# Performance work log

Measured on AMD Instinct MI355X. Metric: run time of the kernel, lower is better.

Reference implementation:

```python
import jax, jax.numpy as jnp
import numpy as np

C = 192; G = 12; CG = C // G          # channels, groups, channels per group
KS = 3; PAD = 1; K = KS * KS - 1      # 3x3 kernel, remove_center=True -> 8 points
HID = 4 * C                           # mlp_ratio = 4
OFFSET_SCALE = 1.0

# kernel dilation grid (x, y) pairs, center removed (remove_center=True)
_pts = np.arange(KS) - (KS - 1) // 2
_gx, _gy = np.meshgrid(_pts, _pts, indexing='ij')
_grid = np.stack([_gx.ravel(), _gy.ravel()], -1).astype(np.float32)
_grid = _grid[~np.all(_grid == 0, axis=1)]   # (K, 2)
GRID = jnp.asarray(_grid)


def _ln(x, w, b, eps=1e-5):
    mu = jnp.mean(x, -1, keepdims=True)
    var = jnp.var(x, -1, keepdims=True)
    return (x - mu) * jax.lax.rsqrt(var + eps) * w + b


def _dcnv3(x, in_proj_w, in_proj_b, dw_w, dw_b, dw_ln_w, dw_ln_b,
           off_w, off_b, mask_w, mask_b, cfs_w, cfs_b, out_proj_w, out_proj_b):
    # x: (B, H, W, C) channels-last
    B, H, W, _ = x.shape
    xp = x @ in_proj_w + in_proj_b          # value / x_proj
    # depthwise conv -> LN -> GELU on the raw input (offset/mask branch)
    x1 = jax.lax.conv_general_dilated(
        x, dw_w, (1, 1), 'SAME',
        dimension_numbers=('NHWC', 'HWIO', 'NHWC'),
        feature_group_count=C) + dw_b
    x1 = jax.nn.gelu(_ln(x1, dw_ln_w, dw_ln_b, 1e-6), approximate=False)
    off = (x1 @ off_w + off_b).reshape(B, H, W, G, K, 2)      # (dx, dy) in pixels
    mask = jax.nn.softmax((x1 @ mask_w + mask_b).reshape(B, H, W, G, K), axis=-1)
    # pad value and flatten spatial; (B, Hp*Wp, G, 1, CG)
    Hp, Wp = H + 2 * PAD, W + 2 * PAD
    v = jnp.pad(xp, ((0, 0), (PAD, PAD), (PAD, PAD), (0, 0))).reshape(B, Hp * Wp, G, 1, CG)
    # sampling locations in padded-image pixel index coords (grid_sample align_corners=False)
    bx = jnp.arange(W, dtype=x.dtype)[None, None, :, None, None] + PAD
    by = jnp.arange(H, dtype=x.dtype)[None, :, None, None, None] + PAD
    px = (bx + (GRID[:, 0] + off[..., 0]) * OFFSET_SCALE).reshape(B, H * W, G, K)
    py = (by + (GRID[:, 1] + off[..., 1]) * OFFSET_SCALE).reshape(B, H * W, G, K)
    x0 = jnp.floor(px); y0 = jnp.floor(py)
    wx = px - x0; wy = py - y0
    ix0 = x0.astype(jnp.int32); iy0 = y0.astype(jnp.int32)

    def gather(iy, ix):
        valid = ((iy >= 0) & (iy < Hp) & (ix >= 0) & (ix < Wp)).astype(x.dtype)
        idx = jnp.clip(iy, 0, Hp - 1) * Wp + jnp.clip(ix, 0, Wp - 1)
        s = jnp.take_along_axis(v, idx[..., None], axis=1)    # (B, HW, G, K, CG)
        return s * valid[..., None]

    s = (gather(iy0, ix0)         * ((1 - wy) * (1 - wx))[..., None]
       + gather(iy0, ix0 + 1)     * ((1 - wy) * wx)[..., None]
       + gather(iy0 + 1, ix0)     * (wy * (1 - wx))[..., None]
       + gather(iy0 + 1, ix0 + 1) * (wy * wx)[..., None])
    out = jnp.einsum('bngk,bngkc->bngc', mask.reshape(B, H * W, G, K), s).reshape(B, H, W, C)
    # center feature scale
    cfs = jax.nn.sigmoid(x1 @ cfs_w.T + cfs_b)                # (B, H, W, G)
    cfs = jnp.repeat(cfs, CG, axis=-1)                        # (B, H, W, C)
    out = out * (1 - cfs) + xp * cfs
    return out @ out_proj_w + out_proj_b


def _forward(x, norm1_w, norm1_b, norm2_w, norm2_b, rpn1_w, rpn1_b, rpn2_w, rpn2_b,
             in_proj_w, in_proj_b, dw_w, dw_b, dw_ln_w, dw_ln_b, off_w, off_b,
             mask_w, mask_b, cfs_w, cfs_b, out_proj_w, out_proj_b,
             fc1_w, fc1_b, fc2_w, fc2_b):
    d = _dcnv3(_ln(x, norm1_w, norm1_b), in_proj_w, in_proj_b, dw_w, dw_b,
               dw_ln_w, dw_ln_b, off_w, off_b, mask_w, mask_b, cfs_w, cfs_b,
               out_proj_w, out_proj_b)
    x = x + _ln(d, rpn1_w, rpn1_b)                            # res_post_norm branch 1
    h = jax.nn.gelu(_ln(x, norm2_w, norm2_b) @ fc1_w + fc1_b, approximate=False) @ fc2_w + fc2_b
    x = x + _ln(h, rpn2_w, rpn2_b)                            # res_post_norm branch 2
    return x


def setup_inputs():
    key = jax.random.key(0)
    ks = jax.random.split(key, 12)
    r = lambda i, shape, s=0.02: jax.random.normal(ks[i], shape, jnp.float32) * s
    B, H, W = 4, 56, 56
    return dict(
        x=jax.random.normal(ks[0], (B, H, W, C), jnp.float32),
        norm1_w=jnp.ones((C,)), norm1_b=jnp.zeros((C,)),
        norm2_w=jnp.ones((C,)), norm2_b=jnp.zeros((C,)),
        rpn1_w=jnp.ones((C,)), rpn1_b=jnp.zeros((C,)),
        rpn2_w=jnp.ones((C,)), rpn2_b=jnp.zeros((C,)),
        in_proj_w=r(1, (C, C)), in_proj_b=jnp.zeros((C,)),
        dw_w=r(2, (KS, KS, 1, C), 0.1), dw_b=jnp.zeros((C,)),
        dw_ln_w=jnp.ones((C,)), dw_ln_b=jnp.zeros((C,)),
        off_w=r(3, (C, G * K * 2), 0.1), off_b=jnp.zeros((G * K * 2,)),
        mask_w=r(4, (C, G * K), 0.1), mask_b=jnp.zeros((G * K,)),
        cfs_w=r(5, (G, C), 0.1), cfs_b=jnp.zeros((G,)),
        out_proj_w=r(6, (C, C)), out_proj_b=jnp.zeros((C,)),
        fc1_w=r(7, (C, HID)), fc1_b=jnp.zeros((HID,)),
        fc2_w=r(8, (HID, C)), fc2_b=jnp.zeros((C,)),
    )


def reference(x, norm1_w, norm1_b, norm2_w, norm2_b, rpn1_w, rpn1_b, rpn2_w, rpn2_b,
              in_proj_w, in_proj_b, dw_w, dw_b, dw_ln_w, dw_ln_b, off_w, off_b,
              mask_w, mask_b, cfs_w, cfs_b, out_proj_w, out_proj_b,
              fc1_w, fc1_b, fc2_w, fc2_b):
    return _forward(x, norm1_w, norm1_b, norm2_w, norm2_b, rpn1_w, rpn1_b, rpn2_w, rpn2_b,
                    in_proj_w, in_proj_b, dw_w, dw_b, dw_ln_w, dw_ln_b, off_w, off_b,
                    mask_w, mask_b, cfs_w, cfs_b, out_proj_w, out_proj_b,
                    fc1_w, fc1_b, fc2_w, fc2_b)
```

## Files before the change

### kernel.cpp

```cpp
#include <hip/hip_runtime.h>
#include <hip/hip_bf16.h>
#include <math.h>


#define BATCH 4
#define HH 56
#define WW 56
#define CC 192
#define NPIX (BATCH * HH * WW)
#define XS_STR 200
#define H1S 776
#define OFS 193
#define MLS 97

typedef __hip_bfloat16 bf16;
typedef __attribute__((ext_vector_type(8))) short short8;
typedef __attribute__((ext_vector_type(4))) float float4v;

__device__ __forceinline__ float gelu_exact(float x) {
    return 0.5f * x * (1.f + erff(x * 0.70710678118654752f));
}
__device__ __forceinline__ bf16 f2b(float f) { return __float2bfloat16(f); }
__device__ __forceinline__ float b2f(bf16 h) { return __bfloat162float(h); }
__device__ __forceinline__ float4 ldb4(const bf16* p) {
    const ushort4 u = *(const ushort4*)p;
    float4 r;
    r.x = __uint_as_float((unsigned)u.x << 16);
    r.y = __uint_as_float((unsigned)u.y << 16);
    r.z = __uint_as_float((unsigned)u.z << 16);
    r.w = __uint_as_float((unsigned)u.w << 16);
    return r;
}
__device__ __forceinline__ void stb4(bf16* p, float4 v) {
    ushort4 u;
    bf16 h;
    h = f2b(v.x); u.x = *(unsigned short*)&h;
    h = f2b(v.y); u.y = *(unsigned short*)&h;
    h = f2b(v.z); u.z = *(unsigned short*)&h;
    h = f2b(v.w); u.w = *(unsigned short*)&h;
    *(ushort4*)p = u;
}

__global__ __launch_bounds__(256) void prep_w_k(const float* __restrict__ inpw,
        const float* __restrict__ offw, const float* __restrict__ maskw,
        const float* __restrict__ outpw, const float* __restrict__ fc1w,
        const float* __restrict__ fc2w, bf16* __restrict__ wsB)
{
    const int i = blockIdx.x * 256 + threadIdx.x;
    bf16* inpP = wsB;
    bf16* omP  = wsB + 36864;
    bf16* outP = wsB + 92160;
    bf16* fc1P = wsB + 129024;
    bf16* fc2P = wsB + 276480;
    const int j   = i & 7;
    const int l   = (i >> 3) & 63;
    const int n15 = l & 15, q = l >> 4;
    const int grp = i >> 9;
    if (i < 36864) {
        const int t = grp / 6, c = grp - t * 6;
        const int n = 16 * t + n15, k = 32 * c + 8 * q + j;
        inpP[i] = f2b(inpw[(size_t)k * 192 + n]);
        outP[i] = f2b(outpw[(size_t)k * 192 + n]);
    }
    if (i < 55296) {
        const int t = grp / 6, c = grp - t * 6;
        const int n = 16 * t + n15, k = 32 * c + 8 * q + j;
        omP[i] = (n < 192) ? f2b(offw[(size_t)k * 192 + n])
                           : f2b(maskw[(size_t)k * 96 + (n - 192)]);
    }
    if (i < 147456) {
        const int t1 = grp / 6, c1 = grp - t1 * 6;
        const int n1 = 16 * t1 + n15, k1 = 32 * c1 + 8 * q + j;
        fc1P[i] = f2b(fc1w[(size_t)k1 * 768 + n1]);
        const int t2 = grp / 24, c2 = grp - t2 * 24;
        const int n2 = 16 * t2 + n15, k2 = 32 * c2 + 8 * q + j;
        fc2P[i] = f2b(fc2w[(size_t)k2 * 192 + n2]);
    }
}

__global__ __launch_bounds__(256) void ln_gemm16_k(const float* __restrict__ x,
        const float* __restrict__ n1w, const float* __restrict__ n1b,
        const bf16* __restrict__ wP, const float* __restrict__ bias,
        bf16* __restrict__ xn_out, bf16* __restrict__ xp_out)
{
    __shared__ __align__(16) bf16 xs[16 * XS_STR];
    const int tid = threadIdx.x;
    const int w   = tid >> 6;
    const int l   = tid & 63;
    const int n15 = l & 15;
    const int q   = l >> 4;
    const int p0  = blockIdx.x * 16;

    #pragma unroll
    for (int rr = 0; rr < 4; rr++) {
        const int lr = 4 * w + rr;
        const size_t base = (size_t)(p0 + lr) * CC;
        float v[3];
        #pragma unroll
        for (int i = 0; i < 3; i++) v[i] = x[base + l + 64 * i];
        float s = v[0] + v[1] + v[2];
        float qq = v[0]*v[0] + v[1]*v[1] + v[2]*v[2];
        #pragma unroll
        for (int off = 32; off > 0; off >>= 1) {
            s  += __shfl_xor(s, off, 64);
            qq += __shfl_xor(qq, off, 64);
        }
        const float mu  = s * (1.f / CC);
        const float var = qq * (1.f / CC) - mu * mu;
        const float rs  = rsqrtf(var + 1e-5f);
        #pragma unroll
        for (int i = 0; i < 3; i++) {
            const int c = l + 64 * i;
            const bf16 h = f2b((v[i] - mu) * rs * n1w[c] + n1b[c]);
            xs[lr * XS_STR + c] = h;
            xn_out[base + c] = h;
        }
    }
    __syncthreads();

    short8 aF[6];
    #pragma unroll
    for (int c = 0; c < 6; c++)
        aF[c] = *(const short8*)&xs[n15 * XS_STR + c * 32 + q * 8];

    #pragma unroll
    for (int t = 0; t < 3; t++) {
        const int tile = 3 * w + t;
        float4v acc = (float4v){0.f, 0.f, 0.f, 0.f};
        #pragma unroll
        for (int c = 0; c < 6; c++) {
            const short8 bF = *(const short8*)&wP[(size_t)((tile * 6 + c) * 64 + l) * 8];
            acc = __builtin_amdgcn_mfma_f32_16x16x32_bf16(aF[c], bF, acc, 0, 0, 0);
        }
        const int n0 = 16 * tile;
        const float bb = bias[n0 + n15];
        #pragma unroll
        for (int r = 0; r < 4; r++)
            xp_out[(size_t)(p0 + 4 * q + r) * 192 + n0 + n15] = f2b(acc[r] + bb);
    }
}

__global__ __launch_bounds__(256) void dwconv_ln_gelu_k(
        const bf16* __restrict__ xn, const float* __restrict__ dww,
        const float* __restrict__ dwb, const float* __restrict__ lnw,
        const float* __restrict__ lnb, bf16* __restrict__ x1)
{
    __shared__ float cv[4][192];
    const int bid  = (blockIdx.x & 7) * (NPIX / 32) + (blockIdx.x >> 3);
    const int t    = threadIdx.x;
    const int ws   = t >> 6;
    const int l    = t & 63;
    const int pix  = bid * 4 + ws;
    const int bimg = pix / (HH * WW);
    const int hw   = pix - bimg * HH * WW;
    const int h    = hw / WW;
    const int wx   = hw - h * WW;

    if (l < 48) {
        const int c0 = l * 4;
        float4 acc = *(const float4*)&dwb[c0];
        #pragma unroll
        for (int ky = 0; ky < 3; ky++) {
            const int yy = h + ky - 1;
            if (yy < 0 || yy >= HH) continue;
            #pragma unroll
            for (int kx = 0; kx < 3; kx++) {
                const int xx = wx + kx - 1;
                if (xx < 0 || xx >= WW) continue;
                const float4 a = ldb4(&xn[((size_t)(bimg * HH + yy) * WW + xx) * CC + c0]);
                const float4 ww = *(const float4*)&dww[(ky * 3 + kx) * CC + c0];
                acc.x += a.x * ww.x; acc.y += a.y * ww.y;
                acc.z += a.z * ww.z; acc.w += a.w * ww.w;
            }
        }
        *(float4*)&cv[ws][c0] = acc;
    }
    __syncthreads();

    float v[3];
    #pragma unroll
    for (int i = 0; i < 3; i++) v[i] = cv[ws][l + 64 * i];
    float s = v[0] + v[1] + v[2];
    float q = v[0]*v[0] + v[1]*v[1] + v[2]*v[2];
    #pragma unroll
    for (int off = 32; off > 0; off >>= 1) {
        s += __shfl_xor(s, off, 64);
        q += __shfl_xor(q, off, 64);
    }
    const float mu  = s * (1.f / CC);
    const float var = q * (1.f / CC) - mu * mu;
    const float rs  = rsqrtf(var + 1e-6f);
    #pragma unroll
    for (int i = 0; i < 3; i++) {
        const int c = l + 64 * i;
        x1[(size_t)pix * CC + c] = f2b(gelu_exact((v[i] - mu) * rs * lnw[c] + lnb[c]));
    }
}

__global__ __launch_bounds__(256) void offmask_sample_k(
        const bf16* __restrict__ xp, const bf16* __restrict__ x1g,
        const bf16* __restrict__ omP, const float* __restrict__ offb,
        const float* __restrict__ maskb, const float* __restrict__ cfsw,
        const float* __restrict__ cfsb, bf16* __restrict__ outb)
{
    __shared__ __align__(16) bf16 xs[8 * XS_STR];
    __shared__ float offs_l[8][OFS];
    __shared__ float mls_l[8][MLS];

    const int tid = threadIdx.x;
    const int w   = tid >> 6;
    const int l   = tid & 63;
    const int n15 = l & 15;
    const int q   = l >> 4;
    const int bid = (blockIdx.x & 7) * (NPIX / 64) + (blockIdx.x >> 3);
    const int p0  = bid * 8;

    for (int i = tid; i < 8 * 24; i += 256) {
        const int px = i / 24, c8 = i - px * 24;
        *(short8*)&xs[px * XS_STR + c8 * 8] = *(const short8*)&x1g[(size_t)(p0 + px) * 192 + c8 * 8];
    }
    __syncthreads();

    {
        short8 aF[6];
        #pragma unroll
        for (int c = 0; c < 6; c++)
            aF[c] = (n15 < 8)
                  ? *(const short8*)&xs[n15 * XS_STR + c * 32 + q * 8]
                  : (short8){0, 0, 0, 0, 0, 0, 0, 0};

        for (int t = w; t < 18; t += 4) {
            float4v acc = (float4v){0.f, 0.f, 0.f, 0.f};
            #pragma unroll
            for (int c = 0; c < 6; c++) {
                const short8 bF = *(const short8*)&omP[(size_t)((t * 6 + c) * 64 + l) * 8];
                acc = __builtin_amdgcn_mfma_f32_16x16x32_bf16(aF[c], bF, acc, 0, 0, 0);
            }
            if (q < 2) {
                const int n0 = 16 * t;
                if (t < 12) {
                    const float bb = offb[n0 + n15];
                    #pragma unroll
                    for (int r = 0; r < 4; r++)
                        offs_l[4 * q + r][n0 + n15] = acc[r] + bb;
                } else {
                    const int m0 = n0 - 192;
                    const float bb = maskb[m0 + n15];
                    #pragma unroll
                    for (int r = 0; r < 4; r++)
                        mls_l[4 * q + r][m0 + n15] = acc[r] + bb;
                }
            }
        }
    }
    __syncthreads();

    #pragma unroll
    for (int it = 0; it < 2; it++) {
        const int id = tid + 256 * it;
        if (id >= 384) break;
        const int px  = id / 48;
        const int s2  = id - px * 48;
        const int g   = s2 >> 2;
        const int c4  = s2 & 3;
        const int ch0 = g * 16 + c4 * 4;
        const int pix = p0 + px;
        const int bimg = pix / (HH * WW);
        const int hw   = pix - bimg * HH * WW;
        const int h    = hw / WW;
        const int wxp  = hw - h * WW;

        float lg[8];
        float mx = -1e30f;
        #pragma unroll
        for (int k = 0; k < 8; k++) { lg[k] = mls_l[px][g * 8 + k]; mx = fmaxf(mx, lg[k]); }
        float se = 0.f;
        #pragma unroll
        for (int k = 0; k < 8; k++) { lg[k] = expf(lg[k] - mx); se += lg[k]; }
        const float inv = 1.f / se;

        const int GX[8] = {-1, -1, -1, 0, 0, 1, 1, 1};
        const int GY[8] = {-1, 0, 1, -1, 1, -1, 0, 1};
        const size_t imgbase = (size_t)bimg * HH * WW * CC;

        float4 acc = {0.f, 0.f, 0.f, 0.f};
        #pragma unroll 2
        for (int k = 0; k < 8; k++) {
            const float px_ = (float)wxp + (float)GX[k] + offs_l[px][g * 16 + 2 * k];
            const float py_ = (float)h   + (float)GY[k] + offs_l[px][g * 16 + 2 * k + 1];
            const float fx = floorf(px_), fy = floorf(py_);
            const float wxf = px_ - fx, wyf = py_ - fy;
            const int x0 = (int)fx, y0 = (int)fy;
            float4 v00 = {0,0,0,0}, v01 = {0,0,0,0}, v10 = {0,0,0,0}, v11 = {0,0,0,0};
            if (y0 >= 0 && y0 < HH) {
                if (x0 >= 0 && x0 < WW)
                    v00 = ldb4(&xp[imgbase + (size_t)(y0 * WW + x0) * CC + ch0]);
                if (x0 + 1 >= 0 && x0 + 1 < WW)
                    v01 = ldb4(&xp[imgbase + (size_t)(y0 * WW + x0 + 1) * CC + ch0]);
            }
            if (y0 + 1 >= 0 && y0 + 1 < HH) {
                if (x0 >= 0 && x0 < WW)
                    v10 = ldb4(&xp[imgbase + (size_t)((y0 + 1) * WW + x0) * CC + ch0]);
                if (x0 + 1 >= 0 && x0 + 1 < WW)
                    v11 = ldb4(&xp[imgbase + (size_t)((y0 + 1) * WW + x0 + 1) * CC + ch0]);
            }
            const float w00 = (1.f - wyf) * (1.f - wxf), w01 = (1.f - wyf) * wxf;
            const float w10 = wyf * (1.f - wxf),         w11 = wyf * wxf;
            const float mk = lg[k] * inv;
            acc.x += mk * (w00 * v00.x + w01 * v01.x + w10 * v10.x + w11 * v11.x);
            acc.y += mk * (w00 * v00.y + w01 * v01.y + w10 * v10.y + w11 * v11.y);
            acc.z += mk * (w00 * v00.z + w01 * v01.z + w10 * v10.z + w11 * v11.z);
            acc.w += mk * (w00 * v00.w + w01 * v01.w + w10 * v10.w + w11 * v11.w);
        }

        float part = 0.f;
        #pragma unroll
        for (int j = 0; j < 48; j++)
            part += b2f(xs[px * XS_STR + 4 * j + c4]) * cfsw[(size_t)g * CC + 4 * j + c4];
        part += __shfl_xor(part, 1, 64);
        part += __shfl_xor(part, 2, 64);
        const float cf = 1.f / (1.f + expf(-(part + cfsb[g])));

        const float4 xpc = ldb4(&xp[(size_t)pix * CC + ch0]);
        float4 o;
        o.x = acc.x * (1.f - cf) + xpc.x * cf;
        o.y = acc.y * (1.f - cf) + xpc.y * cf;
        o.z = acc.z * (1.f - cf) + xpc.z * cf;
        o.w = acc.w * (1.f - cf) + xpc.w * cf;
        stb4(&outb[(size_t)pix * CC + ch0], o);
    }
}

__global__ __launch_bounds__(256) void gemm_ln2_mlp_k(const bf16* __restrict__ A,
        const bf16* __restrict__ wP, const float* __restrict__ bias,
        const float* __restrict__ x,
        const float* __restrict__ r1w, const float* __restrict__ r1b,
        const float* __restrict__ n2w, const float* __restrict__ n2b,
        const bf16* __restrict__ fc1P, const float* __restrict__ fc1b,
        const bf16* __restrict__ fc2P, const float* __restrict__ fc2b,
        const float* __restrict__ r2w, const float* __restrict__ r2b,
        float* __restrict__ out)
{
    __shared__ __align__(16) bf16 xs[16 * XS_STR];
    __shared__ __align__(16) bf16 h1[16 * H1S];
    __shared__ float ps[4][16], pq[4][16], ps2[4][16], pq2[4][16];

    const int tid = threadIdx.x;
    const int w   = tid >> 6;
    const int l   = tid & 63;
    const int n15 = l & 15;
    const int q   = l >> 4;
    const int p0  = blockIdx.x * 16;

    for (int i = tid; i < 16 * 24; i += 256) {
        const int px = i / 24, c8 = i - px * 24;
        *(short8*)&xs[px * XS_STR + c8 * 8] = *(const short8*)&A[(size_t)(p0 + px) * 192 + c8 * 8];
    }
    __syncthreads();

    {
        short8 aF[6];
        #pragma unroll
        for (int c = 0; c < 6; c++)
            aF[c] = *(const short8*)&xs[n15 * XS_STR + c * 32 + q * 8];

        float4v acc[3];
        #pragma unroll
        for (int t = 0; t < 3; t++) {
            const int tile = 3 * w + t;
            acc[t] = (float4v){0.f, 0.f, 0.f, 0.f};
            #pragma unroll
            for (int c = 0; c < 6; c++) {
                const short8 bF = *(const short8*)&wP[(size_t)((tile * 6 + c) * 64 + l) * 8];
                acc[t] = __builtin_amdgcn_mfma_f32_16x16x32_bf16(aF[c], bF, acc[t], 0, 0, 0);
            }
            const float bb = bias[16 * tile + n15];
            #pragma unroll
            for (int r = 0; r < 4; r++) acc[t][r] += bb;
        }

        #pragma unroll
        for (int r = 0; r < 4; r++) {
            float sp = acc[0][r] + acc[1][r] + acc[2][r];
            float qp = acc[0][r]*acc[0][r] + acc[1][r]*acc[1][r] + acc[2][r]*acc[2][r];
            #pragma unroll
            for (int o = 1; o < 16; o <<= 1) {
                sp += __shfl_xor(sp, o, 64);
                qp += __shfl_xor(qp, o, 64);
            }
            if (n15 == 0) { ps[w][4 * q + r] = sp; pq[w][4 * q + r] = qp; }
        }
        __syncthreads();

        float x2v[3][4];
        #pragma unroll
        for (int r = 0; r < 4; r++) {
            const int row = 4 * q + r;
            const float s  = ps[0][row] + ps[1][row] + ps[2][row] + ps[3][row];
            const float qq = pq[0][row] + pq[1][row] + pq[2][row] + pq[3][row];
            const float mu  = s * (1.f / CC);
            const float var = qq * (1.f / CC) - mu * mu;
            const float rs  = rsqrtf(var + 1e-5f);
            const size_t grow = p0 + row;
            #pragma unroll
            for (int t = 0; t < 3; t++) {
                const int col = 48 * w + 16 * t + n15;
                x2v[t][r] = x[grow * CC + col] + (acc[t][r] - mu) * rs * r1w[col] + r1b[col];
            }
        }
        #pragma unroll
        for (int r = 0; r < 4; r++) {
            float sp = x2v[0][r] + x2v[1][r] + x2v[2][r];
            float qp = x2v[0][r]*x2v[0][r] + x2v[1][r]*x2v[1][r] + x2v[2][r]*x2v[2][r];
            #pragma unroll
            for (int o = 1; o < 16; o <<= 1) {
                sp += __shfl_xor(sp, o, 64);
                qp += __shfl_xor(qp, o, 64);
            }
            if (n15 == 0) { ps2[w][4 * q + r] = sp; pq2[w][4 * q + r] = qp; }
        }
        __syncthreads();

        #pragma unroll
        for (int r = 0; r < 4; r++) {
            const int row = 4 * q + r;
            const float s  = ps2[0][row] + ps2[1][row] + ps2[2][row] + ps2[3][row];
            const float qq = pq2[0][row] + pq2[1][row] + pq2[2][row] + pq2[3][row];
            const float mu  = s * (1.f / CC);
            const float var = qq * (1.f / CC) - mu * mu;
            const float rs  = rsqrtf(var + 1e-5f);
            #pragma unroll
            for (int t = 0; t < 3; t++) {
                const int col = 48 * w + 16 * t + n15;
                xs[row * XS_STR + col] = f2b((x2v[t][r] - mu) * rs * n2w[col] + n2b[col]);
            }
        }
        __syncthreads();

        short8 aF2[6];
        #pragma unroll
        for (int c = 0; c < 6; c++)
            aF2[c] = *(const short8*)&xs[n15 * XS_STR + c * 32 + q * 8];

        #pragma unroll
        for (int t1 = 0; t1 < 12; t1++) {
            const int tile = 12 * w + t1;
            float4v a1 = (float4v){0.f, 0.f, 0.f, 0.f};
            #pragma unroll
            for (int c = 0; c < 6; c++) {
                const short8 bF = *(const short8*)&fc1P[(size_t)((tile * 6 + c) * 64 + l) * 8];
                a1 = __builtin_amdgcn_mfma_f32_16x16x32_bf16(aF2[c], bF, a1, 0, 0, 0);
            }
            const int n0 = 16 * tile;
            const float bb = fc1b[n0 + n15];
            #pragma unroll
            for (int r = 0; r < 4; r++)
                h1[(4 * q + r) * H1S + n0 + n15] = f2b(gelu_exact(a1[r] + bb));
        }
        __syncthreads();

        float4v acc2[3];
        #pragma unroll
        for (int t = 0; t < 3; t++) acc2[t] = (float4v){0.f, 0.f, 0.f, 0.f};
        #pragma unroll 4
        for (int kc = 0; kc < 24; kc++) {
            const short8 a2 = *(const short8*)&h1[n15 * H1S + kc * 32 + q * 8];
            #pragma unroll
            for (int t = 0; t < 3; t++) {
                const int tile = 3 * w + t;
                const short8 bF = *(const short8*)&fc2P[(size_t)((tile * 24 + kc) * 64 + l) * 8];
                acc2[t] = __builtin_amdgcn_mfma_f32_16x16x32_bf16(a2, bF, acc2[t], 0, 0, 0);
            }
        }
        #pragma unroll
        for (int t = 0; t < 3; t++) {
            const float bb = fc2b[48 * w + 16 * t + n15];
            #pragma unroll
            for (int r = 0; r < 4; r++) acc2[t][r] += bb;
        }

        #pragma unroll
        for (int r = 0; r < 4; r++) {
            float sp = acc2[0][r] + acc2[1][r] + acc2[2][r];
            float qp = acc2[0][r]*acc2[0][r] + acc2[1][r]*acc2[1][r] + acc2[2][r]*acc2[2][r];
            #pragma unroll
            for (int o = 1; o < 16; o <<= 1) {
                sp += __shfl_xor(sp, o, 64);
                qp += __shfl_xor(qp, o, 64);
            }
            if (n15 == 0) { ps[w][4 * q + r] = sp; pq[w][4 * q + r] = qp; }
        }
        __syncthreads();

        #pragma unroll
        for (int r = 0; r < 4; r++) {
            const int row = 4 * q + r;
            const float s  = ps[0][row] + ps[1][row] + ps[2][row] + ps[3][row];
            const float qq = pq[0][row] + pq[1][row] + pq[2][row] + pq[3][row];
            const float mu  = s * (1.f / CC);
            const float var = qq * (1.f / CC) - mu * mu;
            const float rs  = rsqrtf(var + 1e-5f);
            const size_t grow = p0 + row;
            #pragma unroll
            for (int t = 0; t < 3; t++) {
                const int col = 48 * w + 16 * t + n15;
                out[grow * CC + col] = x2v[t][r]
                                     + (acc2[t][r] - mu) * rs * r2w[col] + r2b[col];
            }
        }
    }
}

extern "C" void kernel_launch(void* const* d_in, const int* in_sizes, int n_in,
                              void* d_out, int out_size, void* d_ws, size_t ws_size,
                              hipStream_t stream) {
    const float* x      = (const float*)d_in[0];
    const float* n1w    = (const float*)d_in[1];
    const float* n1b    = (const float*)d_in[2];
    const float* n2w    = (const float*)d_in[3];
    const float* n2b    = (const float*)d_in[4];
    const float* rpn1w  = (const float*)d_in[5];
    const float* rpn1b  = (const float*)d_in[6];
    const float* rpn2w  = (const float*)d_in[7];
    const float* rpn2b  = (const float*)d_in[8];
    const float* inpw   = (const float*)d_in[9];
    const float* inpb   = (const float*)d_in[10];
    const float* dww    = (const float*)d_in[11];
    const float* dwb    = (const float*)d_in[12];
    const float* dwlnw  = (const float*)d_in[13];
    const float* dwlnb  = (const float*)d_in[14];
    const float* offw   = (const float*)d_in[15];
    const float* offb   = (const float*)d_in[16];
    const float* maskw  = (const float*)d_in[17];
    const float* maskb  = (const float*)d_in[18];
    const float* cfsw   = (const float*)d_in[19];
    const float* cfsb   = (const float*)d_in[20];
    const float* outpw  = (const float*)d_in[21];
    const float* outpb  = (const float*)d_in[22];
    const float* fc1w   = (const float*)d_in[23];
    const float* fc1b   = (const float*)d_in[24];
    const float* fc2w   = (const float*)d_in[25];
    const float* fc2b   = (const float*)d_in[26];

    const int N = NPIX;
    const size_t NP = (size_t)N * CC;
    bf16* B0  = (bf16*)d_ws;
    bf16* B1  = B0 + NP;
    bf16* B3  = B1 + NP;
    bf16* wsB = B3 + NP;
    const bf16* inpP = wsB;
    const bf16* omP  = wsB + 36864;
    const bf16* outP = wsB + 92160;
    const bf16* fc1P = wsB + 129024;
    const bf16* fc2P = wsB + 276480;

    const int lnG = N / 4;
    const int g16 = N / 16;
    const int g8  = N / 8;

    prep_w_k<<<576, 256, 0, stream>>>(inpw, offw, maskw, outpw, fc1w, fc2w, wsB);
    ln_gemm16_k<<<g16, 256, 0, stream>>>(x, n1w, n1b, inpP, inpb, B0, B1);
    dwconv_ln_gelu_k<<<lnG, 256, 0, stream>>>(B0, dww, dwb, dwlnw, dwlnb, B3);
    offmask_sample_k<<<g8, 256, 0, stream>>>(B1, B3, omP, offb, maskb,
                                             cfsw, cfsb, B0);
    gemm_ln2_mlp_k<<<g16, 256, 0, stream>>>(B0, outP, outpb, x, rpn1w, rpn1b,
                                            n2w, n2b, fc1P, fc1b, fc2P, fc2b,
                                            rpn2w, rpn2b, (float*)d_out);
}
```

Before: 210.6 us.

## Fold center-feature-scale into offset/mask MFMA and widen sampling loads to 8 channels

Appends the 12 center-feature-scale weight columns as an extra MFMA tile in the packed offset/mask weight, so the sigmoid gate is computed by the matrix unit instead of a scalar 48-term dot product per thread. Softmax over mask logits moves into the MFMA epilogue using lane shuffles, so the normalized mask is stored in shared memory. The bilinear sampling phase now has each thread handle 8 channels with 16-byte loads, using 192 threads instead of 384 thread-slots. This cuts redundant scalar work and load instructions, at the cost of fewer active threads and more registers per thread in the gather loop.

```diff
diff --git a/kernel.cpp b/kernel.cpp
--- a/kernel.cpp
+++ b/kernel.cpp
@@ -22,6 +22,9 @@
 }
 __device__ __forceinline__ bf16 f2b(float f) { return __float2bfloat16(f); }
 __device__ __forceinline__ float b2f(bf16 h) { return __bfloat162float(h); }
+__device__ __forceinline__ float b2fu(short s) {
+    return __uint_as_float((unsigned)(unsigned short)s << 16);
+}
 __device__ __forceinline__ float4 ldb4(const bf16* p) {
     const ushort4 u = *(const ushort4*)p;
     float4 r;
@@ -43,15 +46,16 @@
 
 __global__ __launch_bounds__(256) void prep_w_k(const float* __restrict__ inpw,
         const float* __restrict__ offw, const float* __restrict__ maskw,
-        const float* __restrict__ outpw, const float* __restrict__ fc1w,
-        const float* __restrict__ fc2w, bf16* __restrict__ wsB)
+        const float* __restrict__ cfsw, const float* __restrict__ outpw,
+        const float* __restrict__ fc1w, const float* __restrict__ fc2w,
+        bf16* __restrict__ wsB)
 {
     const int i = blockIdx.x * 256 + threadIdx.x;
     bf16* inpP = wsB;
     bf16* omP  = wsB + 36864;
-    bf16* outP = wsB + 92160;
-    bf16* fc1P = wsB + 129024;
-    bf16* fc2P = wsB + 276480;
+    bf16* outP = wsB + 95232;
+    bf16* fc1P = wsB + 132096;
+    bf16* fc2P = wsB + 279552;
     const int j   = i & 7;
     const int l   = (i >> 3) & 63;
     const int n15 = l & 15, q = l >> 4;
@@ -62,11 +66,13 @@
         inpP[i] = f2b(inpw[(size_t)k * 192 + n]);
         outP[i] = f2b(outpw[(size_t)k * 192 + n]);
     }
-    if (i < 55296) {
+    if (i < 58368) {
         const int t = grp / 6, c = grp - t * 6;
         const int n = 16 * t + n15, k = 32 * c + 8 * q + j;
         omP[i] = (n < 192) ? f2b(offw[(size_t)k * 192 + n])
-                           : f2b(maskw[(size_t)k * 96 + (n - 192)]);
+               : (n < 288) ? f2b(maskw[(size_t)k * 96 + (n - 192)])
+               : (n < 300) ? f2b(cfsw[(size_t)(n - 288) * 192 + k])
+                           : f2b(0.f);
     }
     if (i < 147456) {
         const int t1 = grp / 6, c1 = grp - t1 * 6;
@@ -200,12 +206,13 @@
 __global__ __launch_bounds__(256) void offmask_sample_k(
         const bf16* __restrict__ xp, const bf16* __restrict__ x1g,
         const bf16* __restrict__ omP, const float* __restrict__ offb,
-        const float* __restrict__ maskb, const float* __restrict__ cfsw,
-        const float* __restrict__ cfsb, bf16* __restrict__ outb)
+        const float* __restrict__ maskb, const float* __restrict__ cfsb,
+        bf16* __restrict__ outb)
 {
     __shared__ __align__(16) bf16 xs[8 * XS_STR];
     __shared__ float offs_l[8][OFS];
     __shared__ float mls_l[8][MLS];
+    __shared__ float cfs_l[8][16];
 
     const int tid = threadIdx.x;
     const int w   = tid >> 6;
@@ -229,61 +236,74 @@
                   ? *(const short8*)&xs[n15 * XS_STR + c * 32 + q * 8]
                   : (short8){0, 0, 0, 0, 0, 0, 0, 0};
 
-        for (int t = w; t < 18; t += 4) {
+        for (int t = w; t < 19; t += 4) {
             float4v acc = (float4v){0.f, 0.f, 0.f, 0.f};
             #pragma unroll
             for (int c = 0; c < 6; c++) {
                 const short8 bF = *(const short8*)&omP[(size_t)((t * 6 + c) * 64 + l) * 8];
                 acc = __builtin_amdgcn_mfma_f32_16x16x32_bf16(aF[c], bF, acc, 0, 0, 0);
             }
-            if (q < 2) {
+            if (t < 12) {
                 const int n0 = 16 * t;
-                if (t < 12) {
-                    const float bb = offb[n0 + n15];
+                const float bb = offb[n0 + n15];
+                if (q < 2) {
                     #pragma unroll
                     for (int r = 0; r < 4; r++)
                         offs_l[4 * q + r][n0 + n15] = acc[r] + bb;
-                } else {
-                    const int m0 = n0 - 192;
-                    const float bb = maskb[m0 + n15];
-                    #pragma unroll
-                    for (int r = 0; r < 4; r++)
-                        mls_l[4 * q + r][m0 + n15] = acc[r] + bb;
                 }
+            } else if (t < 18) {
+                const int m0 = 16 * t - 192;
+                const float bb = maskb[m0 + n15];
+                #pragma unroll
+                for (int r = 0; r < 4; r++) {
+                    const float vv = acc[r] + bb;
+                    float mx = vv;
+                    mx = fmaxf(mx, __shfl_xor(mx, 1, 64));
+                    mx = fmaxf(mx, __shfl_xor(mx, 2, 64));
+                    mx = fmaxf(mx, __shfl_xor(mx, 4, 64));
+                    const float e = expf(vv - mx);
+                    float se = e;
+                    se += __shfl_xor(se, 1, 64);
+                    se += __shfl_xor(se, 2, 64);
+                    se += __shfl_xor(se, 4, 64);
+                    if (q < 2) mls_l[4 * q + r][m0 + n15] = e * (1.f / se);
+                }
+            } else {
+                const float bb = (n15 < 12) ? cfsb[n15] : 0.f;
+                #pragma unroll
+                for (int r = 0; r < 4; r++) {
+                    const float cf = 1.f / (1.f + expf(-(acc[r] + bb)));
+                    if (q < 2 && n15 < 12) cfs_l[4 * q + r][n15] = cf;
+                }
             }
         }
     }
     __syncthreads();
 
-    #pragma unroll
-    for (int it = 0; it < 2; it++) {
-        const int id = tid + 256 * it;
-        if (id >= 384) break;
-        const int px  = id / 48;
-        const int s2  = id - px * 48;
-        const int g   = s2 >> 2;
-        const int c4  = s2 & 3;
-        const int ch0 = g * 16 + c4 * 4;
+    if (tid < 192) {
+        const int px  = tid / 24;
+        const int s2  = tid - px * 24;
+        const int g   = s2 >> 1;
+        const int ch0 = g * 16 + (s2 & 1) * 8;
         const int pix = p0 + px;
         const int bimg = pix / (HH * WW);
         const int hw   = pix - bimg * HH * WW;
         const int h    = hw / WW;
         const int wxp  = hw - h * WW;
 
-        float lg[8];
-        float mx = -1e30f;
-        #pragma unroll
-        for (int k = 0; k < 8; k++) { lg[k] = mls_l[px][g * 8 + k]; mx = fmaxf(mx, lg[k]); }
-        float se = 0.f;
-        #pragma unroll
-        for (int k = 0; k < 8; k++) { lg[k] = expf(lg[k] - mx); se += lg[k]; }
-        const float inv = 1.f / se;
+        float mk[8];
+        #pragma unroll
+        for (int k = 0; k < 8; k++) mk[k] = mls_l[px][g * 8 + k];
+        const float cf = cfs_l[px][g];
 
         const int GX[8] = {-1, -1, -1, 0, 0, 1, 1, 1};
         const int GY[8] = {-1, 0, 1, -1, 1, -1, 0, 1};
         const size_t imgbase = (size_t)bimg * HH * WW * CC;
 
-        float4 acc = {0.f, 0.f, 0.f, 0.f};
+        float acc[8];
+        #pragma unroll
+        for (int j = 0; j < 8; j++) acc[j] = 0.f;
+
         #pragma unroll 2
         for (int k = 0; k < 8; k++) {
             const float px_ = (float)wxp + (float)GX[k] + offs_l[px][g * 16 + 2 * k];
@@ -291,43 +311,38 @@
             const float fx = floorf(px_), fy = floorf(py_);
             const float wxf = px_ - fx, wyf = py_ - fy;
             const int x0 = (int)fx, y0 = (int)fy;
-            float4 v00 = {0,0,0,0}, v01 = {0,0,0,0}, v10 = {0,0,0,0}, v11 = {0,0,0,0};
+            const short8 z8 = {0, 0, 0, 0, 0, 0, 0, 0};
+            short8 v00 = z8, v01 = z8, v10 = z8, v11 = z8;
+            const bool xin0 = (x0 >= 0) && (x0 < WW);
+            const bool xin1 = (x0 + 1 >= 0) && (x0 + 1 < WW);
             if (y0 >= 0 && y0 < HH) {
-                if (x0 >= 0 && x0 < WW)
-                    v00 = ldb4(&xp[imgbase + (size_t)(y0 * WW + x0) * CC + ch0]);
-                if (x0 + 1 >= 0 && x0 + 1 < WW)
-                    v01 = ldb4(&xp[imgbase + (size_t)(y0 * WW + x0 + 1) * CC + ch0]);
+                if (xin0) v00 = *(const short8*)&xp[imgbase + (size_t)(y0 * WW + x0) * CC + ch0];
+                if (xin1) v01 = *(const short8*)&xp[imgbase + (size_t)(y0 * WW + x0 + 1) * CC + ch0];
             }
             if (y0 + 1 >= 0 && y0 + 1 < HH) {
-                if (x0 >= 0 && x0 < WW)
-                    v10 = ldb4(&xp[imgbase + (size_t)((y0 + 1) * WW + x0) * CC + ch0]);
-                if (x0 + 1 >= 0 && x0 + 1 < WW)
-                    v11 = ldb4(&xp[imgbase + (size_t)((y0 + 1) * WW + x0 + 1) * CC + ch0]);
-            }
-            const float w00 = (1.f - wyf) * (1.f - wxf), w01 = (1.f - wyf) * wxf;
-            const float w10 = wyf * (1.f - wxf),         w11 = wyf * wxf;
-            const float mk = lg[k] * inv;
-            acc.x += mk * (w00 * v00.x + w01 * v01.x + w10 * v10.x + w11 * v11.x);
-            acc.y += mk * (w00 * v00.y + w01 * v01.y + w10 * v10.y + w11 * v11.y);
-            acc.z += mk * (w00 * v00.z + w01 * v01.z + w10 * v10.z + w11 * v11.z);
-            acc.w += mk * (w00 * v00.w + w01 * v01.w + w10 * v10.w + w11 * v11.w);
-        }
-
-        float part = 0.f;
-        #pragma unroll
-        for (int j = 0; j < 48; j++)
-            part += b2f(xs[px * XS_STR + 4 * j + c4]) * cfsw[(size_t)g * CC + 4 * j + c4];
-        part += __shfl_xor(part, 1, 64);
-        part += __shfl_xor(part, 2, 64);
-        const float cf = 1.f / (1.f + expf(-(part + cfsb[g])));
-
-        const float4 xpc = ldb4(&xp[(size_t)pix * CC + ch0]);
-        float4 o;
-        o.x = acc.x * (1.f - cf) + xpc.x * cf;
-        o.y = acc.y * (1.f - cf) + xpc.y * cf;
-        o.z = acc.z * (1.f - cf) + xpc.z * cf;
-        o.w = acc.w * (1.f - cf) + xpc.w * cf;
-        stb4(&outb[(size_t)pix * CC + ch0], o);
+                if (xin0) v10 = *(const short8*)&xp[imgbase + (size_t)((y0 + 1) * WW + x0) * CC + ch0];
+                if (xin1) v11 = *(const short8*)&xp[imgbase + (size_t)((y0 + 1) * WW + x0 + 1) * CC + ch0];
+            }
+            const float w00 = mk[k] * (1.f - wyf) * (1.f - wxf);
+            const float w01 = mk[k] * (1.f - wyf) * wxf;
+            const float w10 = mk[k] * wyf * (1.f - wxf);
+            const float w11 = mk[k] * wyf * wxf;
+            #pragma unroll
+            for (int j = 0; j < 8; j++) {
+                acc[j] += w00 * b2fu(v00[j]) + w01 * b2fu(v01[j])
+                        + w10 * b2fu(v10[j]) + w11 * b2fu(v11[j]);
+            }
+        }
+
+        const short8 xv = *(const short8*)&xp[(size_t)pix * CC + ch0];
+        short8 o;
+        #pragma unroll
+        for (int j = 0; j < 8; j++) {
+            const float ov = acc[j] * (1.f - cf) + b2fu(xv[j]) * cf;
+            bf16 hh = f2b(ov);
+            o[j] = *(short*)&hh;
+        }
+        *(short8*)&outb[(size_t)pix * CC + ch0] = o;
     }
 }
 
@@ -550,19 +565,18 @@
     bf16* wsB = B3 + NP;
     const bf16* inpP = wsB;
     const bf16* omP  = wsB + 36864;
-    const bf16* outP = wsB + 92160;
-    const bf16* fc1P = wsB + 129024;
-    const bf16* fc2P = wsB + 276480;
+    const bf16* outP = wsB + 95232;
+    const bf16* fc1P = wsB + 132096;
+    const bf16* fc2P = wsB + 279552;
 
     const int lnG = N / 4;
     const int g16 = N / 16;
     const int g8  = N / 8;
 
-    prep_w_k<<<576, 256, 0, stream>>>(inpw, offw, maskw, outpw, fc1w, fc2w, wsB);
+    prep_w_k<<<576, 256, 0, stream>>>(inpw, offw, maskw, cfsw, outpw, fc1w, fc2w, wsB);
     ln_gemm16_k<<<g16, 256, 0, stream>>>(x, n1w, n1b, inpP, inpb, B0, B1);
     dwconv_ln_gelu_k<<<lnG, 256, 0, stream>>>(B0, dww, dwb, dwlnw, dwlnb, B3);
-    offmask_sample_k<<<g8, 256, 0, stream>>>(B1, B3, omP, offb, maskb,
-                                             cfsw, cfsb, B0);
+    offmask_sample_k<<<g8, 256, 0, stream>>>(B1, B3, omP, offb, maskb, cfsb, B0);
     gemm_ln2_mlp_k<<<g16, 256, 0, stream>>>(B0, outP, outpb, x, rpn1w, rpn1b,
                                             n2w, n2b, fc1P, fc1b, fc2P, fc2b,
                                             rpn2w, rpn2b, (float*)d_out);
```

Result: faster. 190.9 us (-9.4%).
